# Kernel optimization log

Measured on AMD Instinct MI355X. Metric: run time of the kernel, lower is better.

The kernel has to match this reference:

```python
import jax, jax.numpy as jnp
import numpy as np

NUM_LAYERS = 4
UNITS = 512
DX = 8e-6
WAVELENGTHS = np.array([4.5e-7, 5.32e-7, 6.33e-7], dtype=np.float32)
Z_LAYERS = 0.03
Z_PROP = 0.05
NUM_MODES = 16
BASE_IDX = 1  # base_wavelength_idx in source


def setup_inputs() -> dict:
    key = jax.random.key(0)
    k1, k2 = jax.random.split(key)
    C = len(WAVELENGTHS)
    x = jax.random.normal(k1, (NUM_MODES, C, UNITS, UNITS), dtype=jnp.float32)
    # phase = rand(units, units) * pi, one per layer
    phases = jax.random.uniform(k2, (NUM_LAYERS, UNITS, UNITS), dtype=jnp.float32) * np.pi
    # wavelength_coefficients initialized to base_wavelength / wl (learned params)
    base = WAVELENGTHS[BASE_IDX]
    coeffs = jnp.tile(jnp.asarray(base / WAVELENGTHS, dtype=jnp.float32), (NUM_LAYERS, 1))
    lams = jnp.asarray(WAVELENGTHS)
    return {"x": x, "phases": phases, "coeffs": coeffs, "lams": lams}


def _transfer_fn(lams, z, n, dx):
    # Band-limited angular-spectrum transfer function, per wavelength: [C, H, W]
    f = jnp.fft.fftfreq(n, d=dx).astype(jnp.float32)
    fx2 = f[None, :] ** 2 + f[:, None] ** 2          # [H, W]
    arg = (1.0 / lams)[:, None, None] ** 2 - fx2[None]  # [C, H, W]
    valid = arg > 0
    kz = 2.0 * jnp.pi * jnp.sqrt(jnp.where(valid, arg, 0.0))
    return jnp.where(valid, jnp.exp(1j * (kz * z).astype(jnp.float32)), 0.0)


def _propagate(field, Hf):
    # field: [B, C, H, W] complex; Hf: [C, H, W] — batched angular-spectrum step
    return jnp.fft.ifft2(jnp.fft.fft2(field) * Hf[None])


def reference(x, phases, coeffs, lams):
    n = x.shape[-1]
    H_layer = _transfer_fn(lams, Z_LAYERS, n, DX)  # inter-layer propagation
    H_final = _transfer_fn(lams, Z_PROP, n, DX)    # propagation to detector
    field = x.astype(jnp.complex64)
    for l in range(NUM_LAYERS):
        # per-wavelength effective phase: phase * coeff (depth_factor == 1)
        eff = phases[l][None, :, :] * coeffs[l][:, None, None]  # [C, H, W]
        field = field * jnp.exp(1j * eff)[None]
        field = _propagate(field, H_layer)
    field = _propagate(field, H_final)
    return jnp.abs(field) ** 2
```

## Files before the change

kernel.cpp:

```cpp
#include <hip/hip_runtime.h>
#include <math.h>


#define TWOPI_F 6.2831854820251465f
#define RSQ2    0.70710678f
#define NPIX    (48*512*512)

__device__ __forceinline__ float2 cadd(float2 a, float2 b){ return make_float2(a.x+b.x, a.y+b.y); }
__device__ __forceinline__ float2 csub(float2 a, float2 b){ return make_float2(a.x-b.x, a.y-b.y); }
__device__ __forceinline__ float2 cmul(float2 a, float2 b){ return make_float2(a.x*b.x - a.y*b.y, a.x*b.y + a.y*b.x); }

template<int S> __device__ __forceinline__ float2 mul_i(float2 a){
  return (S>0) ? make_float2(-a.y, a.x) : make_float2(a.y, -a.x);
}
template<int S> __device__ __forceinline__ float2 mul_w1(float2 a){
  return (S>0) ? make_float2(RSQ2*(a.x-a.y), RSQ2*(a.x+a.y))
               : make_float2(RSQ2*(a.x+a.y), RSQ2*(a.y-a.x));
}
template<int S> __device__ __forceinline__ float2 mul_w3(float2 a){
  return (S>0) ? make_float2(RSQ2*(-a.x-a.y), RSQ2*(a.x-a.y))
               : make_float2(RSQ2*(a.y-a.x), RSQ2*(-a.x-a.y));
}
template<int S> __device__ __forceinline__ float2 cmul_tw(float2 v, float2 w){
  float wy = (S>0) ? -w.y : w.y;
  return make_float2(v.x*w.x - v.y*wy, v.x*wy + v.y*w.x);
}

template<int S>
__device__ __forceinline__ void dft8(const float2* a, float2* d){
  float2 b0=cadd(a[0],a[4]), b1=cadd(a[1],a[5]), b2=cadd(a[2],a[6]), b3=cadd(a[3],a[7]);
  float2 b4=csub(a[0],a[4]);
  float2 b5=mul_w1<S>(csub(a[1],a[5]));
  float2 b6=mul_i<S> (csub(a[2],a[6]));
  float2 b7=mul_w3<S>(csub(a[3],a[7]));
  float2 c0=cadd(b0,b2), c2=csub(b0,b2);
  float2 c1=cadd(b1,b3), c3=mul_i<S>(csub(b1,b3));
  float2 c4=cadd(b4,b6), c6=csub(b4,b6);
  float2 c5=cadd(b5,b7), c7=mul_i<S>(csub(b5,b7));
  d[0]=cadd(c0,c1); d[1]=csub(c0,c1);
  d[2]=cadd(c2,c3); d[3]=csub(c2,c3);
  d[4]=cadd(c4,c5); d[5]=csub(c4,c5);
  d[6]=cadd(c6,c7); d[7]=csub(c6,c7);
}

__device__ __forceinline__ int SWZR(int i){ return i ^ ((i>>4)&7); }

__device__ __forceinline__ void make_tw(int t, float2* tw0, float2* tw1){
  float sn, cs;
  __sincosf((TWOPI_F/512.0f)*(float)t, &sn, &cs);
  float2 w0 = make_float2(cs, -sn);
  tw0[0] = make_float2(1.0f, 0.0f);
  #pragma unroll
  for(int k=1;k<8;k++) tw0[k] = cmul(tw0[k-1], w0);
  int p = t>>3;
  __sincosf((TWOPI_F/64.0f)*(float)p, &sn, &cs);
  float2 w1 = make_float2(cs, -sn);
  tw1[0] = make_float2(1.0f, 0.0f);
  #pragma unroll
  for(int k=1;k<8;k++) tw1[k] = cmul(tw1[k-1], w1);
}

template<int S>
__device__ __forceinline__ void fft512(float2* a, float2* o, float2* B0, float2* B1, int t,
                                       float scale, const float2* tw0, const float2* tw1){
  const int km[8] = {0,4,2,6,1,5,3,7};
  float2 d[8];
  dft8<S>(a, d);
  #pragma unroll
  for(int k=0;k<8;k++)
    B0[SWZR(8*t+k)] = (k==0) ? d[km[0]] : cmul_tw<S>(d[km[k]], tw0[k]);
  __syncthreads();
  #pragma unroll
  for(int r=0;r<8;r++) a[r] = B0[SWZR(t+64*r)];
  dft8<S>(a, d);
  {
    int p = t>>3, q = t&7;
    #pragma unroll
    for(int k=0;k<8;k++)
      B1[SWZR(q + 64*p + 8*k)] = (k==0) ? d[km[0]] : cmul_tw<S>(d[km[k]], tw1[k]);
  }
  __syncthreads();
  #pragma unroll
  for(int r=0;r<8;r++) a[r] = B1[SWZR(t+64*r)];
  dft8<S>(a, d);
  #pragma unroll
  for(int k=0;k<8;k++) o[k] = make_float2(d[km[k]].x*scale, d[km[k]].y*scale);
}

template<int S, int LD>
__device__ __forceinline__ void fft512_1b(float2* a, float2* o, float2* B, int t,
                                          float scale, const float2* tw0, const float2* tw1){
  const int km[8] = {0,4,2,6,1,5,3,7};
  float2 d[8];
  dft8<S>(a, d);
  #pragma unroll
  for(int k=0;k<8;k++)
    B[(8*t+k)*LD] = (k==0) ? d[km[0]] : cmul_tw<S>(d[km[k]], tw0[k]);
  __syncthreads();
  #pragma unroll
  for(int r=0;r<8;r++) a[r] = B[(t+64*r)*LD];
  __syncthreads();
  dft8<S>(a, d);
  {
    int p = t>>3, q = t&7;
    #pragma unroll
    for(int k=0;k<8;k++)
      B[(q + 64*p + 8*k)*LD] = (k==0) ? d[km[0]] : cmul_tw<S>(d[km[k]], tw1[k]);
  }
  __syncthreads();
  #pragma unroll
  for(int r=0;r<8;r++) a[r] = B[(t+64*r)*LD];
  dft8<S>(a, d);
  #pragma unroll
  for(int k=0;k<8;k++) o[k] = make_float2(d[km[k]].x*scale, d[km[k]].y*scale);
}


struct AccI {
  float2* p;
  __device__ __forceinline__ float2 ld(int i) const { return p[i]; }
  __device__ __forceinline__ void   st(int i, float2 v) const { p[i] = v; }
};
struct AccS {
  float* re; float* im;
  __device__ __forceinline__ float2 ld(int i) const { return make_float2(re[i], im[i]); }
  __device__ __forceinline__ void   st(int i, float2 v) const { re[i]=v.x; im[i]=v.y; }
};


__device__ __forceinline__ float2 phase_of(float kz, float zf){
  float tt = __fmul_rn(kz, zf);
  double dt = (double)tt;
  double q  = rint(dt * 0.15915494309189535);
  double rr = fma(-q, 6.283185307179586, dt);
  float sn, cs; __sincosf((float)rr, &sn, &cs);
  return make_float2(cs, sn);
}

__global__ __launch_bounds__(256) void k_htab(const float* __restrict__ lams,
                                              float2* __restrict__ H1, float2* __restrict__ H12){
  int e = blockIdx.x*256 + threadIdx.x;
  int c = e >> 18, fy = (e>>9)&511, col = e&511;
  const float lam = lams[c];
  const float il  = 1.0f / lam;
  const float il2 = __fmul_rn(il, il);
  const float DEN = (float)(512.0 * 8e-6);
  int   sx  = (col < 256) ? col : col - 512;
  int   sy  = (fy  < 256) ? fy  : fy  - 512;
  float fxv = (float)sx / DEN, fyv = (float)sy / DEN;
  float arg = __fsub_rn(il2, __fadd_rn(__fmul_rn(fxv,fxv), __fmul_rn(fyv,fyv)));
  float2 h1 = make_float2(0.0f,0.0f), h12 = h1;
  if(arg > 0.0f){
    float s  = (float)sqrt((double)arg);
    float kz = __fmul_rn(6.2831854820251465f, s);
    h1  = phase_of(kz, 0.03f);
    h12 = cmul(h1, phase_of(kz, 0.05f));
  }
  H1[e] = h1; H12[e] = h12;
}


template<class Acc>
__global__ __launch_bounds__(256) void k_row_first(
    const float* __restrict__ x, Acc f,
    const float* __restrict__ phases, const float* __restrict__ coeffs)
{
  __shared__ float2 lds[4][2][512];
  const int w = threadIdx.x >> 6, t = threadIdx.x & 63;
  const int img = blockIdx.x, c = img % 3;
  const int row = (blockIdx.y<<2) + w;
  const int base = (img*512 + row)*512;
  const float* ph = phases + row*512;
  const float coeff = coeffs[c];
  float2 tw0[8], tw1[8]; make_tw(t, tw0, tw1);
  float2 a[8], o[8];
  #pragma unroll
  for(int r=0;r<8;r++){
    int i = t + (r<<6);
    float xv = x[base+i];
    float th = __fmul_rn(ph[i], coeff);
    float sn, cs; __sincosf(th, &sn, &cs);
    a[r] = make_float2(xv*cs, xv*sn);
  }
  fft512<-1>(a, o, lds[w][0], lds[w][1], t, 1.0f, tw0, tw1);
  #pragma unroll
  for(int k=0;k<8;k++){ int i=t+(k<<6); f.st(base+i, o[k]); }
}

template<class Acc>
__global__ __launch_bounds__(256) void k_row_mid(
    Acc f, const float* __restrict__ phases, const float* __restrict__ coeffs, int layer)
{
  __shared__ float2 lds[4][2][512];
  const int w = threadIdx.x >> 6, t = threadIdx.x & 63;
  const int img = blockIdx.x, c = img % 3;
  const int row = (blockIdx.y<<2) + w;
  const int base = (img*512 + row)*512;
  const float* ph = phases + (layer*512 + row)*512;
  const float coeff = coeffs[layer*3 + c];
  float2 tw0[8], tw1[8]; make_tw(t, tw0, tw1);
  float2 a[8], o[8];
  float phr[8];
  #pragma unroll
  for(int r=0;r<8;r++){ int i=t+(r<<6); a[r]=f.ld(base+i); phr[r]=ph[i]; }
  fft512<+1>(a, o, lds[w][0], lds[w][1], t, 1.0f/512.0f, tw0, tw1);
  #pragma unroll
  for(int k=0;k<8;k++){
    float th = __fmul_rn(phr[k], coeff);
    float sn, cs; __sincosf(th, &sn, &cs);
    a[k] = cmul(o[k], make_float2(cs, sn));
  }
  fft512<-1>(a, o, lds[w][0], lds[w][1], t, 1.0f, tw0, tw1);
  #pragma unroll
  for(int k=0;k<8;k++){ int i=t+(k<<6); f.st(base+i, o[k]); }
}

template<class Acc>
__global__ __launch_bounds__(256) void k_row_last(
    Acc f, float* __restrict__ out)
{
  __shared__ float2 lds[4][2][512];
  const int w = threadIdx.x >> 6, t = threadIdx.x & 63;
  const int img = blockIdx.x;
  const int row = (blockIdx.y<<2) + w;
  const int base = (img*512 + row)*512;
  float2 tw0[8], tw1[8]; make_tw(t, tw0, tw1);
  float2 a[8], o[8];
  #pragma unroll
  for(int r=0;r<8;r++){ int i=t+(r<<6); a[r]=f.ld(base+i); }
  fft512<+1>(a, o, lds[w][0], lds[w][1], t, 1.0f/512.0f, tw0, tw1);
  #pragma unroll
  for(int k=0;k<8;k++){ int i=t+(k<<6); out[base+i] = o[k].x*o[k].x + o[k].y*o[k].y; }
}


template<class Acc, bool TAB>
__global__ __launch_bounds__(512, 4) void k_col8(
    Acc f, const float2* __restrict__ Htab, const float* __restrict__ lams, float z1, float z2)
{
  __shared__ float2 lds[512][9];
  const int cx = threadIdx.x & 7, t = threadIdx.x >> 3;
  const int img = blockIdx.x, c = img % 3;
  const int col = (blockIdx.y<<3) + cx;
  const int ibase = (img<<18) + col;
  float2 tw0[8], tw1[8]; make_tw(t, tw0, tw1);
  float2 a[8], o[8], h[8];
  #pragma unroll
  for(int r=0;r<8;r++){ int gi = ibase + ((t+(r<<6))<<9); a[r]=f.ld(gi); }
  if(TAB){
    const float2* Hrow = Htab + (c<<18) + col;
    #pragma unroll
    for(int k=0;k<8;k++) h[k] = Hrow[(t+(k<<6))<<9];
  } else {
    const float lam = lams[c];
    const float il  = 1.0f / lam;
    const float il2 = __fmul_rn(il, il);
    const float DEN = (float)(512.0 * 8e-6);
    int   sx  = (col < 256) ? col : col - 512;
    float fxv = (float)sx / DEN;
    float fx2 = __fmul_rn(fxv, fxv);
    #pragma unroll
    for(int k=0;k<8;k++){
      int fy = t + (k<<6);
      int sy = (fy < 256) ? fy : fy - 512;
      float fyv = (float)sy / DEN;
      float arg = __fsub_rn(il2, __fadd_rn(fx2, __fmul_rn(fyv,fyv)));
      h[k] = make_float2(0.0f, 0.0f);
      if(arg > 0.0f){
        float s  = (float)sqrt((double)arg);
        float kz = __fmul_rn(6.2831854820251465f, s);
        h[k] = phase_of(kz, z1);
        if(z2 != 0.0f) h[k] = cmul(h[k], phase_of(kz, z2));
      }
    }
  }
  fft512_1b<-1,9>(a, o, &lds[0][cx], t, 1.0f, tw0, tw1);
  #pragma unroll
  for(int k=0;k<8;k++) a[k] = cmul(o[k], h[k]);
  __syncthreads();
  fft512_1b<+1,9>(a, o, &lds[0][cx], t, 1.0f/512.0f, tw0, tw1);
  #pragma unroll
  for(int k=0;k<8;k++){ int gi = ibase + ((t+(k<<6))<<9); f.st(gi, o[k]); }
}


extern "C" void kernel_launch(void* const* d_in, const int* in_sizes, int n_in,
                              void* d_out, int out_size, void* d_ws, size_t ws_size,
                              hipStream_t stream)
{
  const float* x      = (const float*)d_in[0];
  const float* phases = (const float*)d_in[1];
  const float* coeffs = (const float*)d_in[2];
  const float* lams   = (const float*)d_in[3];
  float* out = (float*)d_out;

  const size_t fldB = (size_t)NPIX*8;
  const size_t splB = (size_t)NPIX*4;
  const size_t tabB = (size_t)3*512*512*8;

  dim3 gA(48,128), bA(256);
  dim3 gB(48,64),  bB(512);

  if(ws_size >= fldB + 2*tabB){
    AccI f { (float2*)d_ws };
    float2* H1  = (float2*)((char*)d_ws + fldB);
    float2* H12 = H1 + 3*512*512;
    k_htab<<<dim3(3*512*512/256), dim3(256), 0, stream>>>(lams, H1, H12);
    k_row_first<AccI><<<gA, bA, 0, stream>>>(x, f, phases, coeffs);
    for(int l=1; l<=3; l++){
      k_col8<AccI,true><<<gB, bB, 0, stream>>>(f, H1, lams, 0.03f, 0.0f);
      k_row_mid<AccI><<<gA, bA, 0, stream>>>(f, phases, coeffs, l);
    }
    k_col8<AccI,true><<<gB, bB, 0, stream>>>(f, H12, lams, 0.03f, 0.0f);
    k_row_last<AccI><<<gA, bA, 0, stream>>>(f, out);
  } else if(ws_size >= splB + 2*tabB){
    AccS f { out, (float*)d_ws };
    float2* H1  = (float2*)((char*)d_ws + splB);
    float2* H12 = H1 + 3*512*512;
    k_htab<<<dim3(3*512*512/256), dim3(256), 0, stream>>>(lams, H1, H12);
    k_row_first<AccS><<<gA, bA, 0, stream>>>(x, f, phases, coeffs);
    for(int l=1; l<=3; l++){
      k_col8<AccS,true><<<gB, bB, 0, stream>>>(f, H1, lams, 0.03f, 0.0f);
      k_row_mid<AccS><<<gA, bA, 0, stream>>>(f, phases, coeffs, l);
    }
    k_col8<AccS,true><<<gB, bB, 0, stream>>>(f, H12, lams, 0.03f, 0.0f);
    k_row_last<AccS><<<gA, bA, 0, stream>>>(f, out);
  } else {
    AccS f { out, (float*)d_ws };
    k_row_first<AccS><<<gA, bA, 0, stream>>>(x, f, phases, coeffs);
    for(int l=1; l<=3; l++){
      k_col8<AccS,false><<<gB, bB, 0, stream>>>(f, nullptr, lams, 0.03f, 0.0f);
      k_row_mid<AccS><<<gA, bA, 0, stream>>>(f, phases, coeffs, l);
    }
    k_col8<AccS,false><<<gB, bB, 0, stream>>>(f, nullptr, lams, 0.03f, 0.05f);
    k_row_last<AccS><<<gA, bA, 0, stream>>>(f, out);
  }
}
```

Baseline: 346.5 us.

## Use wave-local LDS fences in row FFTs and precompute phase masks

Each row FFT is computed by a single 64-lane wavefront, so the block-wide barriers are replaced with s_waitcnt lgkmcnt(0) fences, and one LDS buffer per wave replaces two. This removes block-wide synchronization and halves shared memory per block. The table kernel also precomputes the complex phase masks exp(i*phase*coeff) for all layers and wavelengths, so the row kernels load them instead of evaluating sincos. That uses extra workspace and adds a branch that only runs when the workspace is large enough. Correctness relies on wave-synchronous LDS access ordering within a wavefront.

```diff
diff --git a/kernel.cpp b/kernel.cpp
--- a/kernel.cpp
+++ b/kernel.cpp
@@ -45,6 +45,8 @@
 
 __device__ __forceinline__ int SWZR(int i){ return i ^ ((i>>4)&7); }
 
+__device__ __forceinline__ void lds_fence(){ asm volatile("s_waitcnt lgkmcnt(0)" ::: "memory"); }
+
 __device__ __forceinline__ void make_tw(int t, float2* tw0, float2* tw1){
   float sn, cs;
   __sincosf((TWOPI_F/512.0f)*(float)t, &sn, &cs);
@@ -61,27 +63,29 @@
 }
 
 template<int S>
-__device__ __forceinline__ void fft512(float2* a, float2* o, float2* B0, float2* B1, int t,
-                                       float scale, const float2* tw0, const float2* tw1){
+__device__ __forceinline__ void fft512_wv(float2* a, float2* o, float2* B, int t,
+                                          float scale, const float2* tw0, const float2* tw1){
   const int km[8] = {0,4,2,6,1,5,3,7};
   float2 d[8];
   dft8<S>(a, d);
   #pragma unroll
   for(int k=0;k<8;k++)
-    B0[SWZR(8*t+k)] = (k==0) ? d[km[0]] : cmul_tw<S>(d[km[k]], tw0[k]);
-  __syncthreads();
-  #pragma unroll
-  for(int r=0;r<8;r++) a[r] = B0[SWZR(t+64*r)];
+    B[SWZR(8*t+k)] = (k==0) ? d[0] : cmul_tw<S>(d[km[k]], tw0[k]);
+  lds_fence();
+  #pragma unroll
+  for(int r=0;r<8;r++) a[r] = B[SWZR(t+64*r)];
+  lds_fence();
   dft8<S>(a, d);
   {
     int p = t>>3, q = t&7;
     #pragma unroll
     for(int k=0;k<8;k++)
-      B1[SWZR(q + 64*p + 8*k)] = (k==0) ? d[km[0]] : cmul_tw<S>(d[km[k]], tw1[k]);
-  }
-  __syncthreads();
-  #pragma unroll
-  for(int r=0;r<8;r++) a[r] = B1[SWZR(t+64*r)];
+      B[SWZR(q + 64*p + 8*k)] = (k==0) ? d[0] : cmul_tw<S>(d[km[k]], tw1[k]);
+  }
+  lds_fence();
+  #pragma unroll
+  for(int r=0;r<8;r++) a[r] = B[SWZR(t+64*r)];
+  lds_fence();
   dft8<S>(a, d);
   #pragma unroll
   for(int k=0;k<8;k++) o[k] = make_float2(d[km[k]].x*scale, d[km[k]].y*scale);
@@ -95,7 +99,7 @@
   dft8<S>(a, d);
   #pragma unroll
   for(int k=0;k<8;k++)
-    B[(8*t+k)*LD] = (k==0) ? d[km[0]] : cmul_tw<S>(d[km[k]], tw0[k]);
+    B[(8*t+k)*LD] = (k==0) ? d[0] : cmul_tw<S>(d[km[k]], tw0[k]);
   __syncthreads();
   #pragma unroll
   for(int r=0;r<8;r++) a[r] = B[(t+64*r)*LD];
@@ -105,7 +109,7 @@
     int p = t>>3, q = t&7;
     #pragma unroll
     for(int k=0;k<8;k++)
-      B[(q + 64*p + 8*k)*LD] = (k==0) ? d[km[0]] : cmul_tw<S>(d[km[k]], tw1[k]);
+      B[(q + 64*p + 8*k)*LD] = (k==0) ? d[0] : cmul_tw<S>(d[km[k]], tw1[k]);
   }
   __syncthreads();
   #pragma unroll
@@ -137,10 +141,14 @@
   return make_float2(cs, sn);
 }
 
-__global__ __launch_bounds__(256) void k_htab(const float* __restrict__ lams,
-                                              float2* __restrict__ H1, float2* __restrict__ H12){
+__global__ __launch_bounds__(256) void k_htab(
+    const float* __restrict__ lams, const float* __restrict__ coeffs,
+    const float* __restrict__ phases,
+    float2* __restrict__ H1, float2* __restrict__ H12, float2* __restrict__ P)
+{
   int e = blockIdx.x*256 + threadIdx.x;
-  int c = e >> 18, fy = (e>>9)&511, col = e&511;
+  int c = e >> 18, yx = e & 0x3FFFF;
+  int fy = yx >> 9, col = yx & 511;
   const float lam = lams[c];
   const float il  = 1.0f / lam;
   const float il2 = __fmul_rn(il, il);
@@ -157,60 +165,86 @@
     h12 = cmul(h1, phase_of(kz, 0.05f));
   }
   H1[e] = h1; H12[e] = h12;
-}
-
-
-template<class Acc>
+  if(P){
+    #pragma unroll
+    for(int l=0;l<4;l++){
+      float th = __fmul_rn(phases[(l<<18) + yx], coeffs[l*3 + c]);
+      float sn, cs; __sincosf(th, &sn, &cs);
+      P[((l*3 + c)<<18) + yx] = make_float2(cs, sn);
+    }
+  }
+}
+
+
+template<class Acc, bool PH>
 __global__ __launch_bounds__(256) void k_row_first(
-    const float* __restrict__ x, Acc f,
+    const float* __restrict__ x, Acc f, const float2* __restrict__ P,
     const float* __restrict__ phases, const float* __restrict__ coeffs)
 {
-  __shared__ float2 lds[4][2][512];
+  __shared__ float2 lds[4][512];
   const int w = threadIdx.x >> 6, t = threadIdx.x & 63;
   const int img = blockIdx.x, c = img % 3;
   const int row = (blockIdx.y<<2) + w;
   const int base = (img*512 + row)*512;
-  const float* ph = phases + row*512;
-  const float coeff = coeffs[c];
   float2 tw0[8], tw1[8]; make_tw(t, tw0, tw1);
   float2 a[8], o[8];
-  #pragma unroll
-  for(int r=0;r<8;r++){
-    int i = t + (r<<6);
-    float xv = x[base+i];
-    float th = __fmul_rn(ph[i], coeff);
-    float sn, cs; __sincosf(th, &sn, &cs);
-    a[r] = make_float2(xv*cs, xv*sn);
-  }
-  fft512<-1>(a, o, lds[w][0], lds[w][1], t, 1.0f, tw0, tw1);
+  if(PH){
+    const float2* Pp = P + (c<<18) + row*512;
+    #pragma unroll
+    for(int r=0;r<8;r++){
+      int i = t + (r<<6);
+      float xv = x[base+i];
+      float2 pv = Pp[i];
+      a[r] = make_float2(xv*pv.x, xv*pv.y);
+    }
+  } else {
+    const float* ph = phases + row*512;
+    const float coeff = coeffs[c];
+    #pragma unroll
+    for(int r=0;r<8;r++){
+      int i = t + (r<<6);
+      float xv = x[base+i];
+      float th = __fmul_rn(ph[i], coeff);
+      float sn, cs; __sincosf(th, &sn, &cs);
+      a[r] = make_float2(xv*cs, xv*sn);
+    }
+  }
+  fft512_wv<-1>(a, o, lds[w], t, 1.0f, tw0, tw1);
   #pragma unroll
   for(int k=0;k<8;k++){ int i=t+(k<<6); f.st(base+i, o[k]); }
 }
 
-template<class Acc>
+template<class Acc, bool PH>
 __global__ __launch_bounds__(256) void k_row_mid(
-    Acc f, const float* __restrict__ phases, const float* __restrict__ coeffs, int layer)
-{
-  __shared__ float2 lds[4][2][512];
+    Acc f, const float2* __restrict__ P,
+    const float* __restrict__ phases, const float* __restrict__ coeffs, int layer)
+{
+  __shared__ float2 lds[4][512];
   const int w = threadIdx.x >> 6, t = threadIdx.x & 63;
   const int img = blockIdx.x, c = img % 3;
   const int row = (blockIdx.y<<2) + w;
   const int base = (img*512 + row)*512;
-  const float* ph = phases + (layer*512 + row)*512;
-  const float coeff = coeffs[layer*3 + c];
   float2 tw0[8], tw1[8]; make_tw(t, tw0, tw1);
-  float2 a[8], o[8];
-  float phr[8];
-  #pragma unroll
-  for(int r=0;r<8;r++){ int i=t+(r<<6); a[r]=f.ld(base+i); phr[r]=ph[i]; }
-  fft512<+1>(a, o, lds[w][0], lds[w][1], t, 1.0f/512.0f, tw0, tw1);
-  #pragma unroll
-  for(int k=0;k<8;k++){
-    float th = __fmul_rn(phr[k], coeff);
-    float sn, cs; __sincosf(th, &sn, &cs);
-    a[k] = cmul(o[k], make_float2(cs, sn));
-  }
-  fft512<-1>(a, o, lds[w][0], lds[w][1], t, 1.0f, tw0, tw1);
+  float2 a[8], o[8], pv[8];
+  if(PH){
+    const float2* Pp = P + ((layer*3 + c)<<18) + row*512;
+    #pragma unroll
+    for(int r=0;r<8;r++){ int i=t+(r<<6); a[r]=f.ld(base+i); pv[r]=Pp[i]; }
+  } else {
+    const float* ph = phases + (layer*512 + row)*512;
+    const float coeff = coeffs[layer*3 + c];
+    #pragma unroll
+    for(int r=0;r<8;r++){
+      int i=t+(r<<6); a[r]=f.ld(base+i);
+      float th = __fmul_rn(ph[i], coeff);
+      float sn, cs; __sincosf(th, &sn, &cs);
+      pv[r] = make_float2(cs, sn);
+    }
+  }
+  fft512_wv<+1>(a, o, lds[w], t, 1.0f/512.0f, tw0, tw1);
+  #pragma unroll
+  for(int k=0;k<8;k++) a[k] = cmul(o[k], pv[k]);
+  fft512_wv<-1>(a, o, lds[w], t, 1.0f, tw0, tw1);
   #pragma unroll
   for(int k=0;k<8;k++){ int i=t+(k<<6); f.st(base+i, o[k]); }
 }
@@ -219,7 +253,7 @@
 __global__ __launch_bounds__(256) void k_row_last(
     Acc f, float* __restrict__ out)
 {
-  __shared__ float2 lds[4][2][512];
+  __shared__ float2 lds[4][512];
   const int w = threadIdx.x >> 6, t = threadIdx.x & 63;
   const int img = blockIdx.x;
   const int row = (blockIdx.y<<2) + w;
@@ -228,7 +262,7 @@
   float2 a[8], o[8];
   #pragma unroll
   for(int r=0;r<8;r++){ int i=t+(r<<6); a[r]=f.ld(base+i); }
-  fft512<+1>(a, o, lds[w][0], lds[w][1], t, 1.0f/512.0f, tw0, tw1);
+  fft512_wv<+1>(a, o, lds[w], t, 1.0f/512.0f, tw0, tw1);
   #pragma unroll
   for(int k=0;k<8;k++){ int i=t+(k<<6); out[base+i] = o[k].x*o[k].x + o[k].y*o[k].y; }
 }
@@ -297,19 +331,34 @@
   const size_t fldB = (size_t)NPIX*8;
   const size_t splB = (size_t)NPIX*4;
   const size_t tabB = (size_t)3*512*512*8;
+  const size_t pB   = (size_t)12*512*512*8;
 
   dim3 gA(48,128), bA(256);
   dim3 gB(48,64),  bB(512);
-
-  if(ws_size >= fldB + 2*tabB){
+  dim3 gH(3*512*512/256), bH(256);
+
+  if(ws_size >= fldB + 2*tabB + pB){
     AccI f { (float2*)d_ws };
     float2* H1  = (float2*)((char*)d_ws + fldB);
     float2* H12 = H1 + 3*512*512;
-    k_htab<<<dim3(3*512*512/256), dim3(256), 0, stream>>>(lams, H1, H12);
-    k_row_first<AccI><<<gA, bA, 0, stream>>>(x, f, phases, coeffs);
+    float2* P   = H12 + 3*512*512;
+    k_htab<<<gH, bH, 0, stream>>>(lams, coeffs, phases, H1, H12, P);
+    k_row_first<AccI,true><<<gA, bA, 0, stream>>>(x, f, P, phases, coeffs);
     for(int l=1; l<=3; l++){
       k_col8<AccI,true><<<gB, bB, 0, stream>>>(f, H1, lams, 0.03f, 0.0f);
-      k_row_mid<AccI><<<gA, bA, 0, stream>>>(f, phases, coeffs, l);
+      k_row_mid<AccI,true><<<gA, bA, 0, stream>>>(f, P, phases, coeffs, l);
+    }
+    k_col8<AccI,true><<<gB, bB, 0, stream>>>(f, H12, lams, 0.03f, 0.0f);
+    k_row_last<AccI><<<gA, bA, 0, stream>>>(f, out);
+  } else if(ws_size >= fldB + 2*tabB){
+    AccI f { (float2*)d_ws };
+    float2* H1  = (float2*)((char*)d_ws + fldB);
+    float2* H12 = H1 + 3*512*512;
+    k_htab<<<gH, bH, 0, stream>>>(lams, coeffs, phases, H1, H12, nullptr);
+    k_row_first<AccI,false><<<gA, bA, 0, stream>>>(x, f, nullptr, phases, coeffs);
+    for(int l=1; l<=3; l++){
+      k_col8<AccI,true><<<gB, bB, 0, stream>>>(f, H1, lams, 0.03f, 0.0f);
+      k_row_mid<AccI,false><<<gA, bA, 0, stream>>>(f, nullptr, phases, coeffs, l);
     }
     k_col8<AccI,true><<<gB, bB, 0, stream>>>(f, H12, lams, 0.03f, 0.0f);
     k_row_last<AccI><<<gA, bA, 0, stream>>>(f, out);
@@ -317,20 +366,20 @@
     AccS f { out, (float*)d_ws };
     float2* H1  = (float2*)((char*)d_ws + splB);
     float2* H12 = H1 + 3*512*512;
-    k_htab<<<dim3(3*512*512/256), dim3(256), 0, stream>>>(lams, H1, H12);
-    k_row_first<AccS><<<gA, bA, 0, stream>>>(x, f, phases, coeffs);
+    k_htab<<<gH, bH, 0, stream>>>(lams, coeffs, phases, H1, H12, nullptr);
+    k_row_first<AccS,false><<<gA, bA, 0, stream>>>(x, f, nullptr, phases, coeffs);
     for(int l=1; l<=3; l++){
       k_col8<AccS,true><<<gB, bB, 0, stream>>>(f, H1, lams, 0.03f, 0.0f);
-      k_row_mid<AccS><<<gA, bA, 0, stream>>>(f, phases, coeffs, l);
+      k_row_mid<AccS,false><<<gA, bA, 0, stream>>>(f, nullptr, phases, coeffs, l);
     }
     k_col8<AccS,true><<<gB, bB, 0, stream>>>(f, H12, lams, 0.03f, 0.0f);
     k_row_last<AccS><<<gA, bA, 0, stream>>>(f, out);
   } else {
     AccS f { out, (float*)d_ws };
-    k_row_first<AccS><<<gA, bA, 0, stream>>>(x, f, phases, coeffs);
+    k_row_first<AccS,false><<<gA, bA, 0, stream>>>(x, f, nullptr, phases, coeffs);
     for(int l=1; l<=3; l++){
       k_col8<AccS,false><<<gB, bB, 0, stream>>>(f, nullptr, lams, 0.03f, 0.0f);
-      k_row_mid<AccS><<<gA, bA, 0, stream>>>(f, phases, coeffs, l);
+      k_row_mid<AccS,false><<<gA, bA, 0, stream>>>(f, nullptr, phases, coeffs, l);
     }
     k_col8<AccS,false><<<gB, bB, 0, stream>>>(f, nullptr, lams, 0.03f, 0.05f);
     k_row_last<AccS><<<gA, bA, 0, stream>>>(f, out);
```

Result: slower. 361.7 us (+4.4%).

## Store intermediate complex field in fp16 and use wave-local LDS FFT sync

Applied to the files above, without the earlier changes.

The intermediate complex field in workspace now uses half2 storage instead of float2, which halves global memory traffic for every row and column pass. Row FFTs now use one LDS buffer per wavefront and replace block-wide __syncthreads with s_waitcnt lgkmcnt fences, relying on each row being owned by a single 64-lane wave. The phase sincos in the middle row kernel is computed before the FFT to overlap with loads. fp16 storage across 8 FFT passes risks accuracy loss and range issues (values unnormalized after forward FFT can reach large magnitudes), and the wave-only fence assumes lockstep execution within a wavefront.

```diff
diff --git a/kernel.cpp b/kernel.cpp
--- a/kernel.cpp
+++ b/kernel.cpp
@@ -1,4 +1,5 @@
 #include <hip/hip_runtime.h>
+#include <hip/hip_fp16.h>
 #include <math.h>
 
 
@@ -45,6 +46,8 @@
 
 __device__ __forceinline__ int SWZR(int i){ return i ^ ((i>>4)&7); }
 
+__device__ __forceinline__ void lds_fence(){ asm volatile("s_waitcnt lgkmcnt(0)" ::: "memory"); }
+
 __device__ __forceinline__ void make_tw(int t, float2* tw0, float2* tw1){
   float sn, cs;
   __sincosf((TWOPI_F/512.0f)*(float)t, &sn, &cs);
@@ -61,27 +64,29 @@
 }
 
 template<int S>
-__device__ __forceinline__ void fft512(float2* a, float2* o, float2* B0, float2* B1, int t,
-                                       float scale, const float2* tw0, const float2* tw1){
+__device__ __forceinline__ void fft512_wv(float2* a, float2* o, float2* B, int t,
+                                          float scale, const float2* tw0, const float2* tw1){
   const int km[8] = {0,4,2,6,1,5,3,7};
   float2 d[8];
   dft8<S>(a, d);
   #pragma unroll
   for(int k=0;k<8;k++)
-    B0[SWZR(8*t+k)] = (k==0) ? d[km[0]] : cmul_tw<S>(d[km[k]], tw0[k]);
-  __syncthreads();
-  #pragma unroll
-  for(int r=0;r<8;r++) a[r] = B0[SWZR(t+64*r)];
+    B[SWZR(8*t+k)] = (k==0) ? d[0] : cmul_tw<S>(d[km[k]], tw0[k]);
+  lds_fence();
+  #pragma unroll
+  for(int r=0;r<8;r++) a[r] = B[SWZR(t+64*r)];
+  lds_fence();
   dft8<S>(a, d);
   {
     int p = t>>3, q = t&7;
     #pragma unroll
     for(int k=0;k<8;k++)
-      B1[SWZR(q + 64*p + 8*k)] = (k==0) ? d[km[0]] : cmul_tw<S>(d[km[k]], tw1[k]);
-  }
-  __syncthreads();
-  #pragma unroll
-  for(int r=0;r<8;r++) a[r] = B1[SWZR(t+64*r)];
+      B[SWZR(q + 64*p + 8*k)] = (k==0) ? d[0] : cmul_tw<S>(d[km[k]], tw1[k]);
+  }
+  lds_fence();
+  #pragma unroll
+  for(int r=0;r<8;r++) a[r] = B[SWZR(t+64*r)];
+  lds_fence();
   dft8<S>(a, d);
   #pragma unroll
   for(int k=0;k<8;k++) o[k] = make_float2(d[km[k]].x*scale, d[km[k]].y*scale);
@@ -95,7 +100,7 @@
   dft8<S>(a, d);
   #pragma unroll
   for(int k=0;k<8;k++)
-    B[(8*t+k)*LD] = (k==0) ? d[km[0]] : cmul_tw<S>(d[km[k]], tw0[k]);
+    B[(8*t+k)*LD] = (k==0) ? d[0] : cmul_tw<S>(d[km[k]], tw0[k]);
   __syncthreads();
   #pragma unroll
   for(int r=0;r<8;r++) a[r] = B[(t+64*r)*LD];
@@ -105,7 +110,7 @@
     int p = t>>3, q = t&7;
     #pragma unroll
     for(int k=0;k<8;k++)
-      B[(q + 64*p + 8*k)*LD] = (k==0) ? d[km[0]] : cmul_tw<S>(d[km[k]], tw1[k]);
+      B[(q + 64*p + 8*k)*LD] = (k==0) ? d[0] : cmul_tw<S>(d[km[k]], tw1[k]);
   }
   __syncthreads();
   #pragma unroll
@@ -116,10 +121,10 @@
 }
 
 
-struct AccI {
-  float2* p;
-  __device__ __forceinline__ float2 ld(int i) const { return p[i]; }
-  __device__ __forceinline__ void   st(int i, float2 v) const { p[i] = v; }
+struct AccH {
+  __half2* p;
+  __device__ __forceinline__ float2 ld(int i) const { return __half22float2(p[i]); }
+  __device__ __forceinline__ void   st(int i, float2 v) const { p[i] = __floats2half2_rn(v.x, v.y); }
 };
 struct AccS {
   float* re; float* im;
@@ -165,7 +170,7 @@
     const float* __restrict__ x, Acc f,
     const float* __restrict__ phases, const float* __restrict__ coeffs)
 {
-  __shared__ float2 lds[4][2][512];
+  __shared__ float2 lds[4][512];
   const int w = threadIdx.x >> 6, t = threadIdx.x & 63;
   const int img = blockIdx.x, c = img % 3;
   const int row = (blockIdx.y<<2) + w;
@@ -182,7 +187,7 @@
     float sn, cs; __sincosf(th, &sn, &cs);
     a[r] = make_float2(xv*cs, xv*sn);
   }
-  fft512<-1>(a, o, lds[w][0], lds[w][1], t, 1.0f, tw0, tw1);
+  fft512_wv<-1>(a, o, lds[w], t, 1.0f, tw0, tw1);
   #pragma unroll
   for(int k=0;k<8;k++){ int i=t+(k<<6); f.st(base+i, o[k]); }
 }
@@ -191,7 +196,7 @@
 __global__ __launch_bounds__(256) void k_row_mid(
     Acc f, const float* __restrict__ phases, const float* __restrict__ coeffs, int layer)
 {
-  __shared__ float2 lds[4][2][512];
+  __shared__ float2 lds[4][512];
   const int w = threadIdx.x >> 6, t = threadIdx.x & 63;
   const int img = blockIdx.x, c = img % 3;
   const int row = (blockIdx.y<<2) + w;
@@ -199,18 +204,18 @@
   const float* ph = phases + (layer*512 + row)*512;
   const float coeff = coeffs[layer*3 + c];
   float2 tw0[8], tw1[8]; make_tw(t, tw0, tw1);
-  float2 a[8], o[8];
-  float phr[8];
-  #pragma unroll
-  for(int r=0;r<8;r++){ int i=t+(r<<6); a[r]=f.ld(base+i); phr[r]=ph[i]; }
-  fft512<+1>(a, o, lds[w][0], lds[w][1], t, 1.0f/512.0f, tw0, tw1);
-  #pragma unroll
-  for(int k=0;k<8;k++){
-    float th = __fmul_rn(phr[k], coeff);
+  float2 a[8], o[8], pv[8];
+  #pragma unroll
+  for(int r=0;r<8;r++){
+    int i=t+(r<<6); a[r]=f.ld(base+i);
+    float th = __fmul_rn(ph[i], coeff);
     float sn, cs; __sincosf(th, &sn, &cs);
-    a[k] = cmul(o[k], make_float2(cs, sn));
-  }
-  fft512<-1>(a, o, lds[w][0], lds[w][1], t, 1.0f, tw0, tw1);
+    pv[r] = make_float2(cs, sn);
+  }
+  fft512_wv<+1>(a, o, lds[w], t, 1.0f/512.0f, tw0, tw1);
+  #pragma unroll
+  for(int k=0;k<8;k++) a[k] = cmul(o[k], pv[k]);
+  fft512_wv<-1>(a, o, lds[w], t, 1.0f, tw0, tw1);
   #pragma unroll
   for(int k=0;k<8;k++){ int i=t+(k<<6); f.st(base+i, o[k]); }
 }
@@ -219,7 +224,7 @@
 __global__ __launch_bounds__(256) void k_row_last(
     Acc f, float* __restrict__ out)
 {
-  __shared__ float2 lds[4][2][512];
+  __shared__ float2 lds[4][512];
   const int w = threadIdx.x >> 6, t = threadIdx.x & 63;
   const int img = blockIdx.x;
   const int row = (blockIdx.y<<2) + w;
@@ -228,7 +233,7 @@
   float2 a[8], o[8];
   #pragma unroll
   for(int r=0;r<8;r++){ int i=t+(r<<6); a[r]=f.ld(base+i); }
-  fft512<+1>(a, o, lds[w][0], lds[w][1], t, 1.0f/512.0f, tw0, tw1);
+  fft512_wv<+1>(a, o, lds[w], t, 1.0f/512.0f, tw0, tw1);
   #pragma unroll
   for(int k=0;k<8;k++){ int i=t+(k<<6); out[base+i] = o[k].x*o[k].x + o[k].y*o[k].y; }
 }
@@ -294,30 +299,31 @@
   const float* lams   = (const float*)d_in[3];
   float* out = (float*)d_out;
 
-  const size_t fldB = (size_t)NPIX*8;
+  const size_t fldH = (size_t)NPIX*4;
   const size_t splB = (size_t)NPIX*4;
   const size_t tabB = (size_t)3*512*512*8;
 
   dim3 gA(48,128), bA(256);
   dim3 gB(48,64),  bB(512);
-
-  if(ws_size >= fldB + 2*tabB){
-    AccI f { (float2*)d_ws };
-    float2* H1  = (float2*)((char*)d_ws + fldB);
+  dim3 gH(3*512*512/256), bH(256);
+
+  if(ws_size >= fldH + 2*tabB){
+    AccH f { (__half2*)d_ws };
+    float2* H1  = (float2*)((char*)d_ws + fldH);
     float2* H12 = H1 + 3*512*512;
-    k_htab<<<dim3(3*512*512/256), dim3(256), 0, stream>>>(lams, H1, H12);
-    k_row_first<AccI><<<gA, bA, 0, stream>>>(x, f, phases, coeffs);
+    k_htab<<<gH, bH, 0, stream>>>(lams, H1, H12);
+    k_row_first<AccH><<<gA, bA, 0, stream>>>(x, f, phases, coeffs);
     for(int l=1; l<=3; l++){
-      k_col8<AccI,true><<<gB, bB, 0, stream>>>(f, H1, lams, 0.03f, 0.0f);
-      k_row_mid<AccI><<<gA, bA, 0, stream>>>(f, phases, coeffs, l);
+      k_col8<AccH,true><<<gB, bB, 0, stream>>>(f, H1, lams, 0.03f, 0.0f);
+      k_row_mid<AccH><<<gA, bA, 0, stream>>>(f, phases, coeffs, l);
     }
-    k_col8<AccI,true><<<gB, bB, 0, stream>>>(f, H12, lams, 0.03f, 0.0f);
-    k_row_last<AccI><<<gA, bA, 0, stream>>>(f, out);
+    k_col8<AccH,true><<<gB, bB, 0, stream>>>(f, H12, lams, 0.03f, 0.0f);
+    k_row_last<AccH><<<gA, bA, 0, stream>>>(f, out);
   } else if(ws_size >= splB + 2*tabB){
     AccS f { out, (float*)d_ws };
     float2* H1  = (float2*)((char*)d_ws + splB);
     float2* H12 = H1 + 3*512*512;
-    k_htab<<<dim3(3*512*512/256), dim3(256), 0, stream>>>(lams, H1, H12);
+    k_htab<<<gH, bH, 0, stream>>>(lams, H1, H12);
     k_row_first<AccS><<<gA, bA, 0, stream>>>(x, f, phases, coeffs);
     for(int l=1; l<=3; l++){
       k_col8<AccS,true><<<gB, bB, 0, stream>>>(f, H1, lams, 0.03f, 0.0f);
```

Result: faster. 294.3 us (-15.1%).
